# Kernel optimization log

Measured on AMD Instinct MI355X. Metric: run time of the kernel, lower is better.

Reference implementation:

```python
import jax, jax.numpy as jnp
import numpy as np

B, S, D, H = 2, 2048, 1024, 16
DH = D // H  # dim per head (dim_singl_head)
SCALE = 0.02


def layer_norm(x, g, b, eps=1e-5):
    m = jnp.mean(x, axis=-1, keepdims=True)
    v = jnp.mean((x - m) ** 2, axis=-1, keepdims=True)
    return (x - m) / jnp.sqrt(v + eps) * g + b


def setup_inputs() -> dict:
    key = jax.random.key(0)
    ks = jax.random.split(key, 12)
    return {
        "query": jax.random.normal(ks[0], (B, S, D), jnp.float32),
        "key": jax.random.normal(ks[1], (B, S, D), jnp.float32),
        "value": jax.random.normal(ks[2], (B, S, D), jnp.float32),
        "mask": jax.random.randint(ks[3], (B, S), 0, 2).astype(jnp.int32),
        "Wq": jax.random.normal(ks[4], (D, D), jnp.float32) * SCALE,
        "bq": jnp.zeros((D,), jnp.float32),
        "Wk": jax.random.normal(ks[5], (D, D), jnp.float32) * SCALE,
        "bk": jnp.zeros((D,), jnp.float32),
        "Wv": jax.random.normal(ks[6], (D, D), jnp.float32) * SCALE,
        "bv": jnp.zeros((D,), jnp.float32),
        "g_att": jnp.ones((DH,), jnp.float32),
        "b_att": jnp.zeros((DH,), jnp.float32),
        "Wres": jax.random.normal(ks[7], (D, D), jnp.float32) * SCALE,
        "bres": jnp.zeros((D,), jnp.float32),
        "g_out": jnp.ones((D,), jnp.float32),
        "b_out": jnp.zeros((D,), jnp.float32),
    }


def reference(query, key, value, mask, Wq, bq, Wk, bk, Wv, bv,
              g_att, b_att, Wres, bres, g_out, b_out):
    # split heads: torch's split(dh,-1)+cat(dim=0) == [H,B,S,dh] layout
    def heads(x):
        return x.reshape(B, S, H, DH).transpose(2, 0, 1, 3)  # [H,B,S,dh]

    q = heads(query @ Wq + bq)
    k = heads(key @ Wk + bk)
    v = heads(value @ Wv + bv)

    # additive mask: (1-mask)*-1e9, broadcast [1,B,1,Sk]
    madd = (1.0 - mask.astype(q.dtype))[None, :, None, :] * -1e9

    scores = jnp.einsum('hbqd,hbkd->hbqk', q, k) / np.float32(np.sqrt(DH))
    w = jax.nn.softmax(scores + madd, axis=-1)
    out = jnp.einsum('hbqk,hbkd->hbqd', w, v)

    out = out + q                         # residual_att
    out = layer_norm(out, g_att, b_att)   # per-head LayerNorm on dh

    # concat heads back: [H,B,S,dh] -> [B,S,H*dh]
    out = out.transpose(1, 2, 0, 3).reshape(B, S, D)

    out = out + jnp.tanh(out @ Wres + bres)  # residual_out branch
    out = layer_norm(out, g_out, b_out)      # norm_out
    return jnp.tanh(out)                     # final activation
```

## Files before the change

kernel.cpp:

```cpp
#include <hip/hip_runtime.h>
#include <cstdint>
#include <cstddef>

#define BB 2
#define SS 2048
#define DD 1024
#define HH 16
#define DHH 64
#define MROWS (BB*SS)

typedef short short8 __attribute__((ext_vector_type(8)));
typedef short short4v __attribute__((ext_vector_type(4)));
typedef float floatx4 __attribute__((ext_vector_type(4)));
typedef unsigned int uint2v __attribute__((ext_vector_type(2)));

#define GAS __attribute__((address_space(1)))
#define LAS __attribute__((address_space(3)))

__device__ __forceinline__ float4 ld4(const float* p) { return *(const float4*)p; }

__device__ __forceinline__ short f2bf(float x) {
    unsigned u = __builtin_bit_cast(unsigned, x);
    unsigned r = (u + 0x7fffu + ((u >> 16) & 1u)) >> 16;
    return (short)r;
}

__device__ __forceinline__ unsigned cvtpk(float lo, float hi) {
    unsigned r;
    asm("v_cvt_pk_bf16_f32 %0, %1, %2" : "=v"(r) : "v"(lo), "v"(hi));
    return r;
}

__device__ __forceinline__ void gl_lds16(const short* g, short* l) {
    __builtin_amdgcn_global_load_lds((const GAS unsigned int*)g,
                                     (LAS unsigned int*)l, 16, 0, 0);
}

__global__ __launch_bounds__(256) void convert_kernel(
    const float* __restrict__ s0, const float* __restrict__ s1, const float* __restrict__ s2,
    short* __restrict__ d0, short* __restrict__ d1, short* __restrict__ d2)
{
    const float* s; short* d;
    if (blockIdx.z == 0)      { s = s0; d = d0; }
    else if (blockIdx.z == 1) { s = s1; d = d1; }
    else                      { s = s2; d = d2; }
    size_t idx = ((size_t)blockIdx.x * 256 + threadIdx.x) * 8;
    float4 a = ld4(s + idx);
    float4 b = ld4(s + idx + 4);
    short8 p;
    p[0] = f2bf(a.x); p[1] = f2bf(a.y); p[2] = f2bf(a.z); p[3] = f2bf(a.w);
    p[4] = f2bf(b.x); p[5] = f2bf(b.y); p[6] = f2bf(b.z); p[7] = f2bf(b.w);
    *(short8*)(d + idx) = p;
}

__global__ __launch_bounds__(256) void transpose_w_kernel(
    const float* __restrict__ W0, const float* __restrict__ W1,
    const float* __restrict__ W2, const float* __restrict__ W3,
    short* __restrict__ T0, short* __restrict__ T1,
    short* __restrict__ T2, short* __restrict__ T3)
{
    const float* W; short* T;
    if (blockIdx.z == 0)      { W = W0; T = T0; }
    else if (blockIdx.z == 1) { W = W1; T = T1; }
    else if (blockIdx.z == 2) { W = W2; T = T2; }
    else                      { W = W3; T = T3; }

    __shared__ short tile[64 * 72];
    const int t  = threadIdx.x;
    const int k0 = blockIdx.x * 64, n0 = blockIdx.y * 64;
#pragma unroll
    for (int i = 0; i < 4; i++) {
        int flat = i * 256 + t;
        int row = flat >> 4;
        int c4  = (flat & 15) * 4;
        float4 v = ld4(W + (size_t)(k0 + row) * DD + n0 + c4);
        tile[(c4 + 0) * 72 + row] = f2bf(v.x);
        tile[(c4 + 1) * 72 + row] = f2bf(v.y);
        tile[(c4 + 2) * 72 + row] = f2bf(v.z);
        tile[(c4 + 3) * 72 + row] = f2bf(v.w);
    }
    __syncthreads();
#pragma unroll
    for (int i = 0; i < 4; i++) {
        int flat = i * 256 + t;
        int nrow = flat >> 4;
        int kc   = (flat & 15) * 4;
        short4v pk = *(short4v*)&tile[nrow * 72 + kc];
        *(short4v*)(T + (size_t)(n0 + nrow) * DD + k0 + kc) = pk;
    }
}

__global__ __launch_bounds__(256) void gemm_bf16_kernel(
    const short* __restrict__ A0, const short* __restrict__ A1, const short* __restrict__ A2,
    const short* __restrict__ Bt0, const short* __restrict__ Bt1, const short* __restrict__ Bt2,
    const float* __restrict__ b0, const float* __restrict__ b1, const float* __restrict__ b2,
    float* __restrict__ Cf0, float* __restrict__ Cf1, float* __restrict__ Cf2,
    short* __restrict__ Cb0, short* __restrict__ Cb1, short* __restrict__ Cb2,
    short* __restrict__ Ct0, short* __restrict__ Ct1, short* __restrict__ Ct2,
    float cs0, float cs1, float cs2)
{
    const short* A; const short* Bt; const float* bias;
    float* Cf; short* Cb; short* Ct; float cbs;
    if (blockIdx.z == 0)      { A = A0; Bt = Bt0; bias = b0; Cf = Cf0; Cb = Cb0; Ct = Ct0; cbs = cs0; }
    else if (blockIdx.z == 1) { A = A1; Bt = Bt1; bias = b1; Cf = Cf1; Cb = Cb1; Ct = Ct1; cbs = cs1; }
    else                      { A = A2; Bt = Bt2; bias = b2; Cf = Cf2; Cb = Cb2; Ct = Ct2; cbs = cs2; }

    __shared__ __align__(16) short As[128 * 32];
    __shared__ __align__(16) short Bs[128 * 32];

    const int tid  = threadIdx.x;
    const int lane = tid & 63;
    const int wave = tid >> 6;
    const int quad = lane >> 4;
    const int l15  = lane & 15;
    const int m0 = blockIdx.y * 128;
    const int n0 = blockIdx.x * 128;
    const int wr = (wave >> 1) * 64;
    const int wc = (wave & 1) * 64;

    floatx4 acc[4][4];
#pragma unroll
    for (int mt = 0; mt < 4; mt++)
#pragma unroll
        for (int nt = 0; nt < 4; nt++) acc[mt][nt] = (floatx4)0.0f;

    for (int k0 = 0; k0 < DD; k0 += 32) {
        __syncthreads();
#pragma unroll
        for (int j = 0; j < 2; j++) {
            int chunk = j * 256 + tid;
            int row = chunk >> 2;
            int ch  = chunk & 3;
            gl_lds16(A  + (size_t)(m0 + row) * DD + k0 + ch * 8, &As[chunk * 8]);
            gl_lds16(Bt + (size_t)(n0 + row) * DD + k0 + ch * 8, &Bs[chunk * 8]);
        }
        __syncthreads();

        short8 af[4], bf[4];
#pragma unroll
        for (int mt = 0; mt < 4; mt++)
            af[mt] = *(const short8*)&As[(wr + mt * 16 + l15) * 32 + quad * 8];
#pragma unroll
        for (int nt = 0; nt < 4; nt++)
            bf[nt] = *(const short8*)&Bs[(wc + nt * 16 + l15) * 32 + quad * 8];
#pragma unroll
        for (int mt = 0; mt < 4; mt++)
#pragma unroll
            for (int nt = 0; nt < 4; nt++)
                acc[mt][nt] = __builtin_amdgcn_mfma_f32_16x16x32_bf16(af[mt], bf[nt], acc[mt][nt], 0, 0, 0);
    }

    float biasv[4];
#pragma unroll
    for (int nt = 0; nt < 4; nt++) biasv[nt] = bias[n0 + wc + nt * 16 + l15];

    if (Cf || Cb) {
#pragma unroll
        for (int mt = 0; mt < 4; mt++)
#pragma unroll
            for (int r = 0; r < 4; r++) {
                const int m = m0 + wr + mt * 16 + quad * 4 + r;
                const size_t rowb = (size_t)m * DD + n0 + wc;
#pragma unroll
                for (int nt = 0; nt < 4; nt++) {
                    float v = acc[mt][nt][r] + biasv[nt];
                    if (Cf) Cf[rowb + nt * 16 + l15] = v;
                    if (Cb) Cb[rowb + nt * 16 + l15] = f2bf(v * cbs);
                }
            }
    }
    if (Ct) {
#pragma unroll
        for (int mt = 0; mt < 4; mt++) {
            const int mbase = m0 + wr + mt * 16 + quad * 4;
            const int bb = mbase >> 11;
            const int s0 = mbase & 2047;
#pragma unroll
            for (int nt = 0; nt < 4; nt++) {
                const int c = n0 + wc + nt * 16 + l15;
                short4v pk;
#pragma unroll
                for (int r = 0; r < 4; r++) pk[r] = f2bf(acc[mt][nt][r] + biasv[nt]);
                *(short4v*)(Ct + ((size_t)(bb * 1024 + c)) * SS + s0) = pk;
            }
        }
    }
}

__global__ __launch_bounds__(512, 4) void attn_mfma_kernel(
    const short* __restrict__ Qb, const short* __restrict__ Kb, const short* __restrict__ Vt,
    const float* __restrict__ Qf, const int* __restrict__ mask,
    const float* __restrict__ g_att, const float* __restrict__ b_att,
    float* __restrict__ X, short* __restrict__ Xb)
{
    const int tid  = threadIdx.x;
    const int lane = tid & 63;
    const int wave = tid >> 6;
    const int quad = lane >> 4;
    const int l15  = lane & 15;

    const int h  = blockIdx.y;
    const int b  = blockIdx.z;
    const int q0 = blockIdx.x * 128;
    const int bS = b * SS;

    __shared__ __align__(16) short Ks[2 * 64 * 72];
    __shared__ __align__(16) short Vs[2 * 64 * 72];
    __shared__ __align__(16) short Ps[8 * 16 * 68];
    __shared__ float smadd[2 * 64];

    short8 qf[2];
#pragma unroll
    for (int s = 0; s < 2; s++)
        qf[s] = *(const short8*)(Qb +
            (size_t)(bS + q0 + wave * 16 + l15) * DD + h * 64 + s * 32 + quad * 8);

    floatx4 o[4];
#pragma unroll
    for (int nt = 0; nt < 4; nt++) o[nt] = (floatx4)0.0f;
    float lsum = 0.0f;

    const int srow = tid >> 3;
    const int sch  = tid & 7;

    short8 kreg, vreg;
    float mreg;
    {
        kreg = *(const short8*)(Kb + (size_t)(bS + srow) * DD + h * 64 + sch * 8);
        vreg = *(const short8*)(Vt + (size_t)(b * 1024 + h * 64 + srow) * SS + sch * 8);
        mreg = (tid < 64) ? (float)mask[bS + tid] : 0.0f;
    }

    for (int kt = 0; kt < SS / 64; kt++) {
        const int bufo = (kt & 1) * (64 * 72);
        *(short8*)&Ks[bufo + srow * 72 + sch * 8] = kreg;
        *(short8*)&Vs[bufo + srow * 72 + sch * 8] = vreg;
        if (tid < 64) smadd[(kt & 1) * 64 + tid] = (1.0f - mreg) * -1e9f;

        if (kt < SS / 64 - 1) {
            const int k0n = (kt + 1) * 64;
            kreg = *(const short8*)(Kb + (size_t)(bS + k0n + srow) * DD + h * 64 + sch * 8);
            vreg = *(const short8*)(Vt + (size_t)(b * 1024 + h * 64 + srow) * SS + k0n + sch * 8);
            mreg = (tid < 64) ? (float)mask[bS + k0n + tid] : 0.0f;
        }

        __builtin_amdgcn_s_waitcnt(0xC07F);
        __builtin_amdgcn_s_barrier();

#pragma unroll
        for (int nt = 0; nt < 4; nt++) {
            const float4 mrow = *(const float4*)&smadd[(kt & 1) * 64 + nt * 16 + quad * 4];
            floatx4 acc = (floatx4)0.0f;
#pragma unroll
            for (int s = 0; s < 2; s++) {
                short8 kf = *(const short8*)&Ks[bufo + (nt * 16 + l15) * 72 + s * 32 + quad * 8];
                acc = __builtin_amdgcn_mfma_f32_16x16x32_bf16(kf, qf[s], acc, 0, 0, 0);
            }
            float p0 = __builtin_exp2f(acc[0] + mrow.x);
            float p1 = __builtin_exp2f(acc[1] + mrow.y);
            float p2 = __builtin_exp2f(acc[2] + mrow.z);
            float p3 = __builtin_exp2f(acc[3] + mrow.w);
            lsum += (p0 + p1) + (p2 + p3);
            unsigned w0 = cvtpk(p0, p1);
            unsigned w1 = cvtpk(p2, p3);
            *(uint2v*)&Ps[wave * 1088 + l15 * 68 + nt * 16 + quad * 4] = (uint2v){w0, w1};
        }

#pragma unroll
        for (int s = 0; s < 2; s++) {
            short8 pa = *(const short8*)&Ps[wave * 1088 + l15 * 68 + s * 32 + quad * 8];
#pragma unroll
            for (int nt = 0; nt < 4; nt++) {
                short8 vb = *(const short8*)&Vs[bufo + (nt * 16 + l15) * 72 + s * 32 + quad * 8];
                o[nt] = __builtin_amdgcn_mfma_f32_16x16x32_bf16(pa, vb, o[nt], 0, 0, 0);
            }
        }
    }

    lsum += __shfl_xor(lsum, 16);
    lsum += __shfl_xor(lsum, 32);
    float rlq[4];
#pragma unroll
    for (int r = 0; r < 4; r++)
        rlq[r] = 1.0f / __shfl(lsum, (lane & 48) | (quad * 4 + r));

    float gvv[4], bvv[4];
#pragma unroll
    for (int nt = 0; nt < 4; nt++) { gvv[nt] = g_att[nt * 16 + l15]; bvv[nt] = b_att[nt * 16 + l15]; }

    float x[4][4];
    float sum[4] = {0.f, 0.f, 0.f, 0.f};
#pragma unroll
    for (int r = 0; r < 4; r++) {
        const float rl = rlq[r];
        const int row = q0 + wave * 16 + quad * 4 + r;
        const size_t base = (size_t)(bS + row) * DD + h * 64;
#pragma unroll
        for (int nt = 0; nt < 4; nt++) {
            float xv = o[nt][r] * rl + Qf[base + nt * 16 + l15];
            x[nt][r] = xv;
            sum[r] += xv;
        }
    }
#pragma unroll
    for (int r = 0; r < 4; r++)
#pragma unroll
        for (int off = 1; off < 16; off <<= 1) sum[r] += __shfl_xor(sum[r], off);

    float vsum[4] = {0.f, 0.f, 0.f, 0.f}, mu[4];
#pragma unroll
    for (int r = 0; r < 4; r++) {
        mu[r] = sum[r] * (1.0f / 64.0f);
#pragma unroll
        for (int nt = 0; nt < 4; nt++) { float d = x[nt][r] - mu[r]; vsum[r] += d * d; }
    }
#pragma unroll
    for (int r = 0; r < 4; r++) {
#pragma unroll
        for (int off = 1; off < 16; off <<= 1) vsum[r] += __shfl_xor(vsum[r], off);
        float rstd = rsqrtf(vsum[r] * (1.0f / 64.0f) + 1e-5f);
        const int row = q0 + wave * 16 + quad * 4 + r;
        const size_t base = (size_t)(bS + row) * DD + h * 64;
#pragma unroll
        for (int nt = 0; nt < 4; nt++) {
            float yv = (x[nt][r] - mu[r]) * rstd * gvv[nt] + bvv[nt];
            X[base + nt * 16 + l15] = yv;
            Xb[base + nt * 16 + l15] = f2bf(yv);
        }
    }
}

__global__ __launch_bounds__(256) void lnout_kernel(
    const float* __restrict__ X, const float* __restrict__ Y,
    const float* __restrict__ g, const float* __restrict__ bcoef,
    float* __restrict__ out)
{
    const int r = blockIdx.x;
    const int t = threadIdx.x;
    const size_t base = (size_t)r * DD + (t << 2);
    float4 x = ld4(X + base);
    float4 y = ld4(Y + base);
    float4 z;
    z.x = x.x + tanhf(y.x);
    z.y = x.y + tanhf(y.y);
    z.z = x.z + tanhf(y.z);
    z.w = x.w + tanhf(y.w);

    __shared__ float red[4];
    __shared__ float stats[2];
    const int w = t >> 6;

    float sv = z.x + z.y + z.z + z.w;
#pragma unroll
    for (int off = 32; off > 0; off >>= 1) sv += __shfl_down(sv, off);
    if ((t & 63) == 0) red[w] = sv;
    __syncthreads();
    if (t == 0) stats[0] = (red[0] + red[1] + red[2] + red[3]) * (1.0f / 1024.0f);
    __syncthreads();
    const float mu = stats[0];

    float4 d;
    d.x = z.x - mu; d.y = z.y - mu; d.z = z.z - mu; d.w = z.w - mu;
    float s2 = d.x * d.x + d.y * d.y + d.z * d.z + d.w * d.w;
#pragma unroll
    for (int off = 32; off > 0; off >>= 1) s2 += __shfl_down(s2, off);
    if ((t & 63) == 0) red[w] = s2;
    __syncthreads();
    if (t == 0) stats[1] = rsqrtf((red[0] + red[1] + red[2] + red[3]) * (1.0f / 1024.0f) + 1e-5f);
    __syncthreads();
    const float rstd = stats[1];

    float4 gv = ld4(g + (t << 2));
    float4 bv = ld4(bcoef + (t << 2));
    float4 o;
    o.x = tanhf(d.x * rstd * gv.x + bv.x);
    o.y = tanhf(d.y * rstd * gv.y + bv.y);
    o.z = tanhf(d.z * rstd * gv.z + bv.z);
    o.w = tanhf(d.w * rstd * gv.w + bv.w);
    *(float4*)(out + base) = o;
}

extern "C" void kernel_launch(void* const* d_in, const int* in_sizes, int n_in,
                              void* d_out, int out_size, void* d_ws, size_t ws_size,
                              hipStream_t stream)
{
    const float* query = (const float*)d_in[0];
    const float* key   = (const float*)d_in[1];
    const float* value = (const float*)d_in[2];
    const int*   mask  = (const int*)  d_in[3];
    const float* Wq    = (const float*)d_in[4];
    const float* bq    = (const float*)d_in[5];
    const float* Wk    = (const float*)d_in[6];
    const float* bk    = (const float*)d_in[7];
    const float* Wv    = (const float*)d_in[8];
    const float* bv    = (const float*)d_in[9];
    const float* g_att = (const float*)d_in[10];
    const float* b_att = (const float*)d_in[11];
    const float* Wres  = (const float*)d_in[12];
    const float* bres  = (const float*)d_in[13];
    const float* g_out = (const float*)d_in[14];
    const float* b_out = (const float*)d_in[15];

    const size_t MAT = (size_t)MROWS * DD;
    float* fws = (float*)d_ws;
    float* Qw = fws;
    float* Xw = fws + MAT;
    short* Qb = (short*)(fws + 2 * MAT);
    short* Kb = Qb + MAT;
    short* Vt = Kb + MAT;
    short* qbf = Vt + MAT;
    short* kbf = qbf + MAT;
    short* vbf = kbf + MAT;
    short* Wtq = vbf + MAT;
    short* Wtk = Wtq + DD * DD;
    short* Wtv = Wtk + DD * DD;
    short* Wtr = Wtv + DD * DD;
    short* Xb = qbf;
    float* Yw = (float*)kbf;

    convert_kernel<<<dim3(MAT / 2048, 1, 3), 256, 0, stream>>>(
        query, key, value, qbf, kbf, vbf);

    transpose_w_kernel<<<dim3(16, 16, 4), 256, 0, stream>>>(
        Wq, Wk, Wv, Wres, Wtq, Wtk, Wtv, Wtr);

    gemm_bf16_kernel<<<dim3(8, 32, 3), 256, 0, stream>>>(
        qbf, kbf, vbf, Wtq, Wtk, Wtv, bq, bk, bv,
        Qw, nullptr, nullptr,
        Qb, Kb, nullptr,
        nullptr, nullptr, Vt,
        0.180336884f, 1.0f, 1.0f);

    attn_mfma_kernel<<<dim3(SS / 128, HH, BB), 512, 0, stream>>>(
        Qb, Kb, Vt, Qw, mask, g_att, b_att, Xw, Xb);

    gemm_bf16_kernel<<<dim3(8, 32, 1), 256, 0, stream>>>(
        Xb, Xb, Xb, Wtr, Wtr, Wtr, bres, bres, bres,
        Yw, Yw, Yw, nullptr, nullptr, nullptr, nullptr, nullptr, nullptr,
        1.0f, 1.0f, 1.0f);

    lnout_kernel<<<MROWS, 256, 0, stream>>>(Xw, Yw, g_out, b_out, (float*)d_out);
}
```

Baseline: 286.1 us.

## Switch attention to 32x32x16 MFMA with register-resident P via permlane32 swap

Rewrites the attention inner loop to use 32x32x16 bf16 MFMA tiles with 4 waves of 32 query rows each, in place of 8 waves of 16 rows. The exp'd score tile is converted to the PV-MFMA A-operand layout in registers with v_permlane32_swap, which removes the per-wave LDS P scratch buffer along with its store/load round trip. The block shrinks to 256 threads, and the LayerNorm epilogue is restructured for the new accumulator layout. This trades fewer LDS ops and better MFMA efficiency against higher register pressure per wave and less latency hiding per block.

New measurement: 290.3 us. Within noise of the previous version (+1.5%).

```diff
diff --git a/kernel.cpp b/kernel.cpp
--- a/kernel.cpp
+++ b/kernel.cpp
@@ -12,7 +12,8 @@
 typedef short short8 __attribute__((ext_vector_type(8)));
 typedef short short4v __attribute__((ext_vector_type(4)));
 typedef float floatx4 __attribute__((ext_vector_type(4)));
-typedef unsigned int uint2v __attribute__((ext_vector_type(2)));
+typedef float floatx16 __attribute__((ext_vector_type(16)));
+typedef unsigned int uint4v __attribute__((ext_vector_type(4)));
 
 #define GAS __attribute__((address_space(1)))
 #define LAS __attribute__((address_space(3)))
@@ -187,7 +188,7 @@
     }
 }
 
-__global__ __launch_bounds__(512, 4) void attn_mfma_kernel(
+__global__ __launch_bounds__(256, 2) void attn_mfma_kernel(
     const short* __restrict__ Qb, const short* __restrict__ Kb, const short* __restrict__ Vt,
     const float* __restrict__ Qf, const int* __restrict__ mask,
     const float* __restrict__ g_att, const float* __restrict__ b_att,
@@ -196,8 +197,8 @@
     const int tid  = threadIdx.x;
     const int lane = tid & 63;
     const int wave = tid >> 6;
-    const int quad = lane >> 4;
-    const int l15  = lane & 15;
+    const int hi   = lane >> 5;
+    const int c    = lane & 31;
 
     const int h  = blockIdx.y;
     const int b  = blockIdx.z;
@@ -206,41 +207,52 @@
 
     __shared__ __align__(16) short Ks[2 * 64 * 72];
     __shared__ __align__(16) short Vs[2 * 64 * 72];
-    __shared__ __align__(16) short Ps[8 * 16 * 68];
     __shared__ float smadd[2 * 64];
 
-    short8 qf[2];
-#pragma unroll
-    for (int s = 0; s < 2; s++)
-        qf[s] = *(const short8*)(Qb +
-            (size_t)(bS + q0 + wave * 16 + l15) * DD + h * 64 + s * 32 + quad * 8);
-
-    floatx4 o[4];
-#pragma unroll
-    for (int nt = 0; nt < 4; nt++) o[nt] = (floatx4)0.0f;
+    short8 qf[4];
+#pragma unroll
+    for (int ks = 0; ks < 4; ks++)
+        qf[ks] = *(const short8*)(Qb +
+            (size_t)(bS + q0 + wave * 32 + c) * DD + h * 64 + ks * 16 + hi * 8);
+
+    floatx16 o[2];
+    o[0] = (floatx16)0.0f;
+    o[1] = (floatx16)0.0f;
     float lsum = 0.0f;
 
     const int srow = tid >> 3;
     const int sch  = tid & 7;
 
-    short8 kreg, vreg;
+    short8 kreg[2], vreg[2];
     float mreg;
     {
-        kreg = *(const short8*)(Kb + (size_t)(bS + srow) * DD + h * 64 + sch * 8);
-        vreg = *(const short8*)(Vt + (size_t)(b * 1024 + h * 64 + srow) * SS + sch * 8);
+#pragma unroll
+        for (int i = 0; i < 2; i++) {
+            int row = srow + i * 32;
+            kreg[i] = *(const short8*)(Kb + (size_t)(bS + row) * DD + h * 64 + sch * 8);
+            vreg[i] = *(const short8*)(Vt + (size_t)(b * 1024 + h * 64 + row) * SS + sch * 8);
+        }
         mreg = (tid < 64) ? (float)mask[bS + tid] : 0.0f;
     }
 
     for (int kt = 0; kt < SS / 64; kt++) {
         const int bufo = (kt & 1) * (64 * 72);
-        *(short8*)&Ks[bufo + srow * 72 + sch * 8] = kreg;
-        *(short8*)&Vs[bufo + srow * 72 + sch * 8] = vreg;
+#pragma unroll
+        for (int i = 0; i < 2; i++) {
+            int row = srow + i * 32;
+            *(short8*)&Ks[bufo + row * 72 + sch * 8] = kreg[i];
+            *(short8*)&Vs[bufo + row * 72 + sch * 8] = vreg[i];
+        }
         if (tid < 64) smadd[(kt & 1) * 64 + tid] = (1.0f - mreg) * -1e9f;
 
         if (kt < SS / 64 - 1) {
             const int k0n = (kt + 1) * 64;
-            kreg = *(const short8*)(Kb + (size_t)(bS + k0n + srow) * DD + h * 64 + sch * 8);
-            vreg = *(const short8*)(Vt + (size_t)(b * 1024 + h * 64 + srow) * SS + k0n + sch * 8);
+#pragma unroll
+            for (int i = 0; i < 2; i++) {
+                int row = srow + i * 32;
+                kreg[i] = *(const short8*)(Kb + (size_t)(bS + k0n + row) * DD + h * 64 + sch * 8);
+                vreg[i] = *(const short8*)(Vt + (size_t)(b * 1024 + h * 64 + row) * SS + k0n + sch * 8);
+            }
             mreg = (tid < 64) ? (float)mask[bS + k0n + tid] : 0.0f;
         }
 
@@ -248,85 +260,74 @@
         __builtin_amdgcn_s_barrier();
 
 #pragma unroll
-        for (int nt = 0; nt < 4; nt++) {
-            const float4 mrow = *(const float4*)&smadd[(kt & 1) * 64 + nt * 16 + quad * 4];
-            floatx4 acc = (floatx4)0.0f;
-#pragma unroll
-            for (int s = 0; s < 2; s++) {
-                short8 kf = *(const short8*)&Ks[bufo + (nt * 16 + l15) * 72 + s * 32 + quad * 8];
-                acc = __builtin_amdgcn_mfma_f32_16x16x32_bf16(kf, qf[s], acc, 0, 0, 0);
-            }
-            float p0 = __builtin_exp2f(acc[0] + mrow.x);
-            float p1 = __builtin_exp2f(acc[1] + mrow.y);
-            float p2 = __builtin_exp2f(acc[2] + mrow.z);
-            float p3 = __builtin_exp2f(acc[3] + mrow.w);
-            lsum += (p0 + p1) + (p2 + p3);
-            unsigned w0 = cvtpk(p0, p1);
-            unsigned w1 = cvtpk(p2, p3);
-            *(uint2v*)&Ps[wave * 1088 + l15 * 68 + nt * 16 + quad * 4] = (uint2v){w0, w1};
-        }
-
-#pragma unroll
-        for (int s = 0; s < 2; s++) {
-            short8 pa = *(const short8*)&Ps[wave * 1088 + l15 * 68 + s * 32 + quad * 8];
-#pragma unroll
-            for (int nt = 0; nt < 4; nt++) {
-                short8 vb = *(const short8*)&Vs[bufo + (nt * 16 + l15) * 72 + s * 32 + quad * 8];
-                o[nt] = __builtin_amdgcn_mfma_f32_16x16x32_bf16(pa, vb, o[nt], 0, 0, 0);
-            }
-        }
-    }
-
-    lsum += __shfl_xor(lsum, 16);
+        for (int g = 0; g < 2; g++) {
+            floatx16 acc = (floatx16)0.0f;
+#pragma unroll
+            for (int ks = 0; ks < 4; ks++) {
+                short8 kf = *(const short8*)&Ks[bufo + (g * 32 + c) * 72 + ks * 16 + hi * 8];
+                acc = __builtin_amdgcn_mfma_f32_32x32x16_bf16(kf, qf[ks], acc, 0, 0, 0);
+            }
+            float p[16];
+#pragma unroll
+            for (int a = 0; a < 4; a++) {
+                float4 mr = *(const float4*)&smadd[(kt & 1) * 64 + g * 32 + a * 8 + hi * 4];
+                p[4 * a + 0] = __builtin_exp2f(acc[4 * a + 0] + mr.x);
+                p[4 * a + 1] = __builtin_exp2f(acc[4 * a + 1] + mr.y);
+                p[4 * a + 2] = __builtin_exp2f(acc[4 * a + 2] + mr.z);
+                p[4 * a + 3] = __builtin_exp2f(acc[4 * a + 3] + mr.w);
+            }
+            lsum += ((p[0] + p[1]) + (p[2] + p[3])) + ((p[4] + p[5]) + (p[6] + p[7]))
+                  + ((p[8] + p[9]) + (p[10] + p[11])) + ((p[12] + p[13]) + (p[14] + p[15]));
+
+#pragma unroll
+            for (int t = 0; t < 2; t++) {
+                unsigned w0 = cvtpk(p[8 * t + 0], p[8 * t + 1]);
+                unsigned w1 = cvtpk(p[8 * t + 2], p[8 * t + 3]);
+                unsigned w2 = cvtpk(p[8 * t + 4], p[8 * t + 5]);
+                unsigned w3 = cvtpk(p[8 * t + 6], p[8 * t + 7]);
+                asm volatile("v_permlane32_swap_b32 %0, %1" : "+v"(w0), "+v"(w2));
+                asm volatile("v_permlane32_swap_b32 %0, %1" : "+v"(w1), "+v"(w3));
+                uint4v u = {w0, w1, w2, w3};
+                short8 pa = __builtin_bit_cast(short8, u);
+#pragma unroll
+                for (int dg = 0; dg < 2; dg++) {
+                    short8 vb = *(const short8*)&Vs[bufo + (dg * 32 + c) * 72
+                                                    + (g * 2 + t) * 16 + hi * 8];
+                    o[dg] = __builtin_amdgcn_mfma_f32_32x32x16_bf16(pa, vb, o[dg], 0, 0, 0);
+                }
+            }
+        }
+    }
+
     lsum += __shfl_xor(lsum, 32);
-    float rlq[4];
-#pragma unroll
-    for (int r = 0; r < 4; r++)
-        rlq[r] = 1.0f / __shfl(lsum, (lane & 48) | (quad * 4 + r));
-
-    float gvv[4], bvv[4];
-#pragma unroll
-    for (int nt = 0; nt < 4; nt++) { gvv[nt] = g_att[nt * 16 + l15]; bvv[nt] = b_att[nt * 16 + l15]; }
-
-    float x[4][4];
-    float sum[4] = {0.f, 0.f, 0.f, 0.f};
-#pragma unroll
-    for (int r = 0; r < 4; r++) {
-        const float rl = rlq[r];
-        const int row = q0 + wave * 16 + quad * 4 + r;
+    const float rl = 1.0f / lsum;
+
+    const float g0v = g_att[c], g1v = g_att[32 + c];
+    const float b0v = b_att[c], b1v = b_att[32 + c];
+
+#pragma unroll
+    for (int r = 0; r < 16; r++) {
+        const int rloc = (r & 3) + 8 * (r >> 2) + 4 * hi;
+        const float rlr = __shfl(rl, rloc);
+        const int row = q0 + wave * 32 + rloc;
         const size_t base = (size_t)(bS + row) * DD + h * 64;
-#pragma unroll
-        for (int nt = 0; nt < 4; nt++) {
-            float xv = o[nt][r] * rl + Qf[base + nt * 16 + l15];
-            x[nt][r] = xv;
-            sum[r] += xv;
-        }
-    }
-#pragma unroll
-    for (int r = 0; r < 4; r++)
-#pragma unroll
-        for (int off = 1; off < 16; off <<= 1) sum[r] += __shfl_xor(sum[r], off);
-
-    float vsum[4] = {0.f, 0.f, 0.f, 0.f}, mu[4];
-#pragma unroll
-    for (int r = 0; r < 4; r++) {
-        mu[r] = sum[r] * (1.0f / 64.0f);
-#pragma unroll
-        for (int nt = 0; nt < 4; nt++) { float d = x[nt][r] - mu[r]; vsum[r] += d * d; }
-    }
-#pragma unroll
-    for (int r = 0; r < 4; r++) {
-#pragma unroll
-        for (int off = 1; off < 16; off <<= 1) vsum[r] += __shfl_xor(vsum[r], off);
-        float rstd = rsqrtf(vsum[r] * (1.0f / 64.0f) + 1e-5f);
-        const int row = q0 + wave * 16 + quad * 4 + r;
-        const size_t base = (size_t)(bS + row) * DD + h * 64;
-#pragma unroll
-        for (int nt = 0; nt < 4; nt++) {
-            float yv = (x[nt][r] - mu[r]) * rstd * gvv[nt] + bvv[nt];
-            X[base + nt * 16 + l15] = yv;
-            Xb[base + nt * 16 + l15] = f2bf(yv);
-        }
+        float x0 = o[0][r] * rlr + Qf[base + c];
+        float x1 = o[1][r] * rlr + Qf[base + 32 + c];
+        float s = x0 + x1;
+#pragma unroll
+        for (int off = 1; off < 32; off <<= 1) s += __shfl_xor(s, off);
+        const float mu = s * (1.0f / 64.0f);
+        float d0 = x0 - mu, d1 = x1 - mu;
+        float v = d0 * d0 + d1 * d1;
+#pragma unroll
+        for (int off = 1; off < 32; off <<= 1) v += __shfl_xor(v, off);
+        const float rstd = rsqrtf(v * (1.0f / 64.0f) + 1e-5f);
+        float y0 = d0 * rstd * g0v + b0v;
+        float y1 = d1 * rstd * g1v + b1v;
+        X[base + c]      = y0;
+        X[base + 32 + c] = y1;
+        Xb[base + c]      = f2bf(y0);
+        Xb[base + 32 + c] = f2bf(y1);
     }
 }
 
@@ -431,7 +432,7 @@
         nullptr, nullptr, Vt,
         0.180336884f, 1.0f, 1.0f);
 
-    attn_mfma_kernel<<<dim3(SS / 128, HH, BB), 512, 0, stream>>>(
+    attn_mfma_kernel<<<dim3(SS / 128, HH, BB), 256, 0, stream>>>(
         Qb, Kb, Vt, Qw, mask, g_att, b_att, Xw, Xb);
 
     gemm_bf16_kernel<<<dim3(8, 32, 1), 256, 0, stream>>>(
```
